# Kernel optimization log

Hardware: AMD Instinct MI355X
Metric: run time of the kernel (lower is better)

The kernel has to match this reference:

```python
import jax, jax.numpy as jnp
import numpy as np

D_MODEL = 1024
NUM_HEADS = 16
D_KEY = 64
CTX = 2048
B, T = 2, 2048


def setup_inputs() -> dict:
    key = jax.random.key(0)
    ks = jax.random.split(key, 5)
    scale_in = 1.0 / np.sqrt(D_MODEL)
    scale_out = 1.0 / np.sqrt(NUM_HEADS * D_KEY)
    return {
        "X": jax.random.normal(ks[0], (B, T, D_MODEL), dtype=jnp.float32),
        "Wqkv": jax.random.uniform(ks[1], (D_MODEL, 3 * NUM_HEADS * D_KEY), dtype=jnp.float32, minval=-scale_in, maxval=scale_in),
        "bqkv": jax.random.uniform(ks[2], (3 * NUM_HEADS * D_KEY,), dtype=jnp.float32, minval=-scale_in, maxval=scale_in),
        "Wout": jax.random.uniform(ks[3], (NUM_HEADS * D_KEY, D_MODEL), dtype=jnp.float32, minval=-scale_out, maxval=scale_out),
        "bout": jax.random.uniform(ks[4], (D_MODEL,), dtype=jnp.float32, minval=-scale_out, maxval=scale_out),
    }


def reference(X, Wqkv, bqkv, Wout, bout):
    b, t, _ = X.shape
    # project and split into q, k, v: [B,T,3,H,Dk]
    qkv = (X @ Wqkv + bqkv).reshape(b, t, 3, NUM_HEADS, D_KEY)
    q = qkv[:, :, 0].transpose(0, 2, 1, 3)  # [B,H,T,Dk]
    k = qkv[:, :, 1].transpose(0, 2, 1, 3)
    v = qkv[:, :, 2].transpose(0, 2, 1, 3)
    scores = jnp.einsum("bhqd,bhkd->bhqk", q, k) / jnp.sqrt(jnp.float32(D_KEY))
    causal = jnp.tril(jnp.ones((t, t), dtype=bool))  # [T,T]
    scores = jnp.where(causal, scores, -jnp.inf)
    attn = jax.nn.softmax(scores, axis=-1)
    out = jnp.einsum("bhqk,bhkd->bhqd", attn, v)  # [B,H,T,Dk]
    out = out.transpose(0, 2, 1, 3).reshape(b, t, NUM_HEADS * D_KEY)
    return out @ Wout + bout
```

## Files before the change

kernel.cpp:

```cpp
#include <hip/hip_runtime.h>
#include <hip/hip_bf16.h>
#include <math.h>

static constexpr int Bc = 2, Hc = 16, Tc = 2048, DKc = 64, DMc = 1024, NQKV = 3072;
#define QSCALE 0.18033688011112042f

typedef unsigned short u16;
typedef unsigned int u32;
typedef short s8v __attribute__((ext_vector_type(8)));
typedef float f32x4 __attribute__((ext_vector_type(4)));
typedef float f32x16 __attribute__((ext_vector_type(16)));
typedef int i32x4 __attribute__((ext_vector_type(4)));

#define DEVINL __device__ __forceinline__

DEVINL u16 f2b(float f) {
    union { float f; unsigned u; } v; v.f = f;
    unsigned u = v.u;
    unsigned r = (u + 0x7fffu + ((u >> 16) & 1u)) >> 16;
    return (u16)r;
}

DEVINL u32 pkbf16(float lo, float up) {
    u32 r;
    asm volatile("v_cvt_pk_bf16_f32 %0, %1, %2" : "=v"(r) : "v"(lo), "v"(up));
    return r;
}

DEVINL float vexp2(float x) {
    float r;
    asm("v_exp_f32 %0, %1" : "=v"(r) : "v"(x));
    return r;
}

DEVINL void pl32swap(u32& a, u32& b) {
    asm volatile("v_permlane32_swap_b32 %0, %1" : "+v"(a), "+v"(b));
}

DEVINL void gl_lds(const void* g, void* l) {
    __builtin_amdgcn_global_load_lds(
        (const __attribute__((address_space(1))) unsigned int*)g,
        (__attribute__((address_space(3))) unsigned int*)l, 16, 0, 0);
}

DEVINL s8v as_s8v(i32x4 x) { union { i32x4 i; s8v v; } u; u.i = x; return u.v; }

DEVINL void transw_tile(const float* __restrict__ W, u16* __restrict__ Wt,
                        int N, int K, int n0, int k0, u16 (*LT)[72], int t) {
    const int rr = t >> 4, cc = (t & 15) * 4;
    #pragma unroll
    for (int it = 0; it < 4; it++) {
        const int row = it * 16 + rr;
        float4 f = *(const float4*)&W[(size_t)(k0 + row) * N + n0 + cc];
        union { u16 u[4]; uint2 d; } o;
        o.u[0] = f2b(f.x); o.u[1] = f2b(f.y); o.u[2] = f2b(f.z); o.u[3] = f2b(f.w);
        *(uint2*)&LT[row][cc] = o.d;
    }
    __syncthreads();
    #pragma unroll
    for (int it = 0; it < 4; it++) {
        const int nrow = it * 16 + rr;
        union { u16 u[4]; uint2 d; } o;
        #pragma unroll
        for (int j = 0; j < 4; j++) o.u[j] = LT[cc + j][nrow];
        *(uint2*)&Wt[(size_t)(n0 + nrow) * K + k0 + cc] = o.d;
    }
}

__global__ __launch_bounds__(256) void prepass(
    const float* __restrict__ X, u16* __restrict__ Xb,
    const float* __restrict__ Wqkv, u16* __restrict__ Wt1,
    const float* __restrict__ Wout, u16* __restrict__ Wt2)
{
    __shared__ u16 LT[64][72];
    const int bid = blockIdx.x, t = threadIdx.x;
    if (bid < 1024) {
        const int n4 = (Bc * Tc * DMc) / 4;
        for (int i = bid * 256 + t; i < n4; i += 1024 * 256) {
            float4 f = ((const float4*)X)[i];
            union { u16 u[4]; uint2 d; } o;
            o.u[0] = f2b(f.x); o.u[1] = f2b(f.y); o.u[2] = f2b(f.z); o.u[3] = f2b(f.w);
            ((uint2*)Xb)[i] = o.d;
        }
    } else if (bid < 1024 + 768) {
        const int b2 = bid - 1024;
        transw_tile(Wqkv, Wt1, NQKV, DMc, (b2 % 48) * 64, (b2 / 48) * 64, LT, t);
    } else {
        const int b2 = bid - 1792;
        transw_tile(Wout, Wt2, DMc, DMc, (b2 % 16) * 64, (b2 / 16) * 64, LT, t);
    }
}

template <int EPI>
__global__ __launch_bounds__(512, 4) void gemm_ks(
    const u16* __restrict__ A, const u16* __restrict__ Bt,
    const float* __restrict__ bias,
    u16* __restrict__ q_out, u16* __restrict__ k_out, u16* __restrict__ v_out,
    float* __restrict__ f_out, int M, int N, int K, int ntn)
{
    __shared__ __align__(16) char Lds[70656];
    const int tid = threadIdx.x, lane = tid & 63, w = tid >> 6;
    const int qd = gridDim.x >> 3;
    const int wg = (blockIdx.x & 7) * qd + (blockIdx.x >> 3);
    const int m0 = (wg / ntn) * 128, n0 = (wg % ntn) * 128;
    const int g = w >> 2, sub = w & 3;
    const int wgm = sub >> 1, wgn = sub & 1;

    f32x4 acc[4][4] = {};
    const int R = K >> 6;

    const int srow = tid >> 2;
    const int skc  = ((tid & 3) ^ ((srow >> 1) & 3)) * 8;

#define STG2(j_) do {                                                          \
        const int ta_ = 2 * (j_), tb_ = ta_ + 1;                               \
        gl_lds(A  + (size_t)(m0 + srow) * K + ta_ * 32 + skc,                  \
               Lds + (ta_ & 3) * 8192 + w * 1024);                             \
        gl_lds(Bt + (size_t)(n0 + srow) * K + ta_ * 32 + skc,                  \
               Lds + 32768 + (ta_ & 3) * 8192 + w * 1024);                     \
        gl_lds(A  + (size_t)(m0 + srow) * K + tb_ * 32 + skc,                  \
               Lds + (tb_ & 3) * 8192 + w * 1024);                             \
        gl_lds(Bt + (size_t)(n0 + srow) * K + tb_ * 32 + skc,                  \
               Lds + 32768 + (tb_ & 3) * 8192 + w * 1024);                     \
    } while (0)
#define BARX() do { __builtin_amdgcn_sched_barrier(0);                         \
        __builtin_amdgcn_s_barrier();                                          \
        __builtin_amdgcn_sched_barrier(0); } while (0)

    STG2(0);
    for (int r = 0; r < R; ++r) {
        if (r + 1 < R) {
            STG2(r + 1);
            asm volatile("s_waitcnt vmcnt(4)" ::: "memory");
        } else {
            asm volatile("s_waitcnt vmcnt(0)" ::: "memory");
        }
        BARX();
        const int sl = (2 * r + g) & 3;
        const char* Abase = Lds + sl * 8192;
        const char* Bbase = Lds + 32768 + sl * 8192;
        s8v af[4], bf[4];
        #pragma unroll
        for (int mi = 0; mi < 4; mi++) {
            const int row = wgm * 64 + mi * 16 + (lane & 15);
            const int s16 = (lane >> 4) ^ ((row >> 1) & 3);
            af[mi] = *(const s8v*)(Abase + row * 64 + s16 * 16);
        }
        #pragma unroll
        for (int ni = 0; ni < 4; ni++) {
            const int row = wgn * 64 + ni * 16 + (lane & 15);
            const int s16 = (lane >> 4) ^ ((row >> 1) & 3);
            bf[ni] = *(const s8v*)(Bbase + row * 64 + s16 * 16);
        }
        __builtin_amdgcn_s_setprio(1);
        #pragma unroll
        for (int mi = 0; mi < 4; mi++)
            #pragma unroll
            for (int ni = 0; ni < 4; ni++)
                acc[mi][ni] = __builtin_amdgcn_mfma_f32_16x16x32_bf16(
                    af[mi], bf[ni], acc[mi][ni], 0, 0, 0);
        __builtin_amdgcn_s_setprio(0);
        BARX();
    }
#undef STG2
#undef BARX

    if (g == 1) {
        char* dst = Lds + sub * 17408 + lane * 272;
        #pragma unroll
        for (int mi = 0; mi < 4; mi++)
            #pragma unroll
            for (int ni = 0; ni < 4; ni++)
                *(f32x4*)(dst + (mi * 4 + ni) * 16) = acc[mi][ni];
    }
    __syncthreads();
    if (g == 0) {
        const char* src = Lds + sub * 17408 + lane * 272;
        #pragma unroll
        for (int mi = 0; mi < 4; mi++)
            #pragma unroll
            for (int ni = 0; ni < 4; ni++)
                acc[mi][ni] += *(const f32x4*)(src + (mi * 4 + ni) * 16);

        #pragma unroll
        for (int mi = 0; mi < 4; mi++)
        #pragma unroll
        for (int ni = 0; ni < 4; ni++)
        #pragma unroll
        for (int r = 0; r < 4; r++) {
            const int row = m0 + wgm * 64 + mi * 16 + (lane >> 4) * 4 + r;
            const int col = n0 + wgn * 64 + ni * 16 + (lane & 15);
            const float val = acc[mi][ni][r] + bias[col];
            if constexpr (EPI == 0) {
                const int sel = col >> 10, rem = col & 1023;
                const int h = rem >> 6, d = rem & 63;
                const int b = row >> 11, tt = row & 2047;
                const size_t idx = ((size_t)(b * Hc + h) * Tc + tt) * DKc + d;
                if (sel == 0) q_out[idx] = f2b(val * QSCALE);
                else if (sel == 1) k_out[idx] = f2b(val);
                else v_out[idx] = f2b(val);
            } else {
                f_out[(size_t)row * N + col] = val;
            }
        }
    }
}

template <int EPI>
__global__ __launch_bounds__(512) void gemm_cv(
    const u16* __restrict__ A, const u16* __restrict__ Bt,
    const float* __restrict__ bias,
    u16* __restrict__ q_out, u16* __restrict__ k_out, u16* __restrict__ v_out,
    float* __restrict__ f_out, int M, int N, int K, int ntn)
{
    __shared__ __align__(16) u16 Al[2][128 * 32];
    __shared__ __align__(16) u16 Bl[2][128 * 32];
    const int tid = threadIdx.x, lane = tid & 63, w = tid >> 6;
    const int qd = gridDim.x >> 3;
    const int wg = (blockIdx.x & 7) * qd + (blockIdx.x >> 3);
    const int m0 = (wg / ntn) * 128, n0 = (wg % ntn) * 128;
    const int wm = w >> 2, wn = w & 3;

    f32x4 acc[4][2] = {};
    const int nt = K >> 5;

    const int srow = tid >> 2;
    const int skc  = ((tid & 3) ^ ((srow >> 1) & 3)) * 8;

#define STG(t_, s_) do {                                                       \
        const int kk_ = (t_) << 5;                                             \
        gl_lds(A + (size_t)(m0 + srow) * K + kk_ + skc,                        \
               (char*)&Al[s_][0] + w * 1024);                                  \
        gl_lds(Bt + (size_t)(n0 + srow) * K + kk_ + skc,                       \
               (char*)&Bl[s_][0] + w * 1024);                                  \
    } while (0)
#define BARX() do { __builtin_amdgcn_sched_barrier(0);                         \
        __builtin_amdgcn_s_barrier();                                          \
        __builtin_amdgcn_sched_barrier(0); } while (0)

    STG(0, 0);
    int buf = 0;
    for (int t = 0; t < nt; t++) {
        if (t + 1 < nt) {
            STG(t + 1, buf ^ 1);
            asm volatile("s_waitcnt vmcnt(2)" ::: "memory");
        } else {
            asm volatile("s_waitcnt vmcnt(0)" ::: "memory");
        }
        BARX();
        s8v af[4], bf[2];
        #pragma unroll
        for (int mi = 0; mi < 4; mi++) {
            const int row = wm * 64 + mi * 16 + (lane & 15);
            const int slot = (lane >> 4) ^ ((row >> 1) & 3);
            af[mi] = *(const s8v*)((const char*)&Al[buf][0] + row * 64 + slot * 16);
        }
        #pragma unroll
        for (int ni = 0; ni < 2; ni++) {
            const int row = wn * 32 + ni * 16 + (lane & 15);
            const int slot = (lane >> 4) ^ ((row >> 1) & 3);
            bf[ni] = *(const s8v*)((const char*)&Bl[buf][0] + row * 64 + slot * 16);
        }
        #pragma unroll
        for (int mi = 0; mi < 4; mi++)
            #pragma unroll
            for (int ni = 0; ni < 2; ni++)
                acc[mi][ni] = __builtin_amdgcn_mfma_f32_16x16x32_bf16(af[mi], bf[ni], acc[mi][ni], 0, 0, 0);
        BARX();
        buf ^= 1;
    }
#undef STG
#undef BARX

    #pragma unroll
    for (int mi = 0; mi < 4; mi++)
    #pragma unroll
    for (int ni = 0; ni < 2; ni++)
    #pragma unroll
    for (int r = 0; r < 4; r++) {
        const int row = m0 + wm * 64 + mi * 16 + (lane >> 4) * 4 + r;
        const int col = n0 + wn * 32 + ni * 16 + (lane & 15);
        const float val = acc[mi][ni][r] + bias[col];
        if constexpr (EPI == 0) {
            const int sel = col >> 10, rem = col & 1023;
            const int h = rem >> 6, d = rem & 63;
            const int b = row >> 11, tt = row & 2047;
            const size_t idx = ((size_t)(b * Hc + h) * Tc + tt) * DKc + d;
            if (sel == 0) q_out[idx] = f2b(val * QSCALE);
            else if (sel == 1) k_out[idx] = f2b(val);
            else v_out[idx] = f2b(val);
        } else {
            f_out[(size_t)row * N + col] = val;
        }
    }
}

__global__ __launch_bounds__(512) void attn_fwd(
    const u16* __restrict__ Q, const u16* __restrict__ K,
    const u16* __restrict__ V, u16* __restrict__ O)
{
    __shared__ __align__(16) char Gl[2][2][2][8192];

    const int bid = blockIdx.x;
    const int bh = bid & 31;
    const int qt = 15 - (bid >> 5);
    const int tid = threadIdx.x;
    const int g = tid >> 8;
    const int gtid = tid & 255;
    const int lane = tid & 63;
    const int ws = (tid >> 6) & 3;
    const int hi = lane >> 5, lq = lane & 31;
    const int q0w = qt * 128 + ws * 32;
    const int qg = q0w + lq;

    const u16* Qb = Q + (size_t)bh * (Tc * DKc);
    const u16* Kb = K + (size_t)bh * (Tc * DKc);
    const u16* Vb = V + (size_t)bh * (Tc * DKc);

    s8v qf[4];
    #pragma unroll
    for (int st = 0; st < 4; st++)
        qf[st] = *(const s8v*)(Qb + (size_t)qg * 64 + st * 16 + hi * 8);

    f32x16 o0 = {}, o1 = {}, lacc = {};

    const int dtw = (q0w + 31) >> 6;
    const int h = qt + 1;
    const int t0 = g * h;

    char* const Kbase = &Gl[g][0][0][0];
    char* const Vbase = &Gl[g][1][0][0];

    const int d2 = (gtid & 31) * 2, kb8 = gtid >> 5;
    const unsigned vsw0 = ((unsigned)(d2 & 7)) << 4;
    const unsigned vsw1 = ((unsigned)((d2 + 1) & 7)) << 4;
    const unsigned ksw = ((unsigned)(lq & 7)) << 4;

    u32 vx[8];

#define ISSUE_K(kt_, dst_) do {                                              \
        const char* Ktile_ = (const char*)(Kb + (size_t)(kt_) * 4096);       \
        _Pragma("unroll")                                                    \
        for (int s_ = 0; s_ < 2; s_++) {                                     \
            const int o_ = s_ * 4096 + gtid * 16;                            \
            const int rk_ = o_ >> 7;                                         \
            const int cb_ = (o_ & 127) ^ ((rk_ & 7) << 4);                   \
            gl_lds(Ktile_ + rk_ * 128 + cb_, (dst_) + s_ * 4096 + ws * 1024); \
        }                                                                    \
    } while (0)

#define LOAD_V(kt_) do {                                                     \
        const u16* Vtile_ = Vb + (size_t)(kt_) * 4096;                       \
        _Pragma("unroll")                                                    \
        for (int i_ = 0; i_ < 8; i_++)                                       \
            vx[i_] = *(const u32*)(Vtile_ + (kb8 * 8 + i_) * 64 + d2);       \
    } while (0)

#define WRITE_V(dst_) do {                                                   \
        s8v v0_, v1_;                                                        \
        _Pragma("unroll")                                                    \
        for (int i_ = 0; i_ < 8; i_++) {                                     \
            v0_[i_] = (short)(vx[i_] & 0xffff);                              \
            v1_[i_] = (short)(vx[i_] >> 16);                                 \
        }                                                                    \
        *(s8v*)((dst_) + d2 * 128 + (((unsigned)(kb8 * 16)) ^ vsw0)) = v0_;  \
        *(s8v*)((dst_) + (d2 + 1) * 128 + (((unsigned)(kb8 * 16)) ^ vsw1)) = v1_; \
    } while (0)

    ISSUE_K(t0, Kbase);
    LOAD_V(t0);
    WRITE_V(Vbase);
    __syncthreads();

    int c = 0;
    for (int i = 0; i < h; i++) {
        const int tki = t0 + i;
        const bool pf_next = (i + 1 < h);
        if (pf_next) {
            ISSUE_K(tki + 1, Kbase + (c ^ 1) * 8192);
            LOAD_V(tki + 1);
        }

        if (tki <= dtw) {
            const char* Kc = Kbase + c * 8192;
            const char* Vc = Vbase + c * 8192;
            f32x16 s0v = {}, s1v = {};
            __builtin_amdgcn_s_setprio(1);
            #pragma unroll
            for (int st = 0; st < 4; st++) {
                const unsigned cbs = (unsigned)(st * 32 + hi * 16);
                s8v kf0 = *(const s8v*)(Kc + lq * 128 + (cbs ^ ksw));
                s8v kf1 = *(const s8v*)(Kc + (32 + lq) * 128 + (cbs ^ ksw));
                s0v = __builtin_amdgcn_mfma_f32_32x32x16_bf16(kf0, qf[st], s0v, 0, 0, 0);
                s1v = __builtin_amdgcn_mfma_f32_32x32x16_bf16(kf1, qf[st], s1v, 0, 0, 0);
            }
            __builtin_amdgcn_s_setprio(0);

            if (tki == dtw) {
                #pragma unroll
                for (int r = 0; r < 16; r++) {
                    const int kg = tki * 64 + (r & 3) + 8 * (r >> 2) + 4 * hi;
                    if (kg > qg) s0v[r] = -INFINITY;
                    if (kg + 32 > qg) s1v[r] = -INFINITY;
                }
            }

            #pragma unroll
            for (int r = 0; r < 16; r++) {
                s0v[r] = vexp2(s0v[r]);
                s1v[r] = vexp2(s1v[r]);
            }
            lacc += s0v;
            lacc += s1v;

            i32x4 pf[4];
            #pragma unroll
            for (int gq = 0; gq < 2; gq++) {
                #pragma unroll
                for (int hq = 0; hq < 2; hq++) {
                    const int base = hq * 8;
                    u32 a0, a1, b0, b1;
                    if (gq == 0) {
                        a0 = pkbf16(s0v[base + 0], s0v[base + 1]);
                        a1 = pkbf16(s0v[base + 2], s0v[base + 3]);
                        b0 = pkbf16(s0v[base + 4], s0v[base + 5]);
                        b1 = pkbf16(s0v[base + 6], s0v[base + 7]);
                    } else {
                        a0 = pkbf16(s1v[base + 0], s1v[base + 1]);
                        a1 = pkbf16(s1v[base + 2], s1v[base + 3]);
                        b0 = pkbf16(s1v[base + 4], s1v[base + 5]);
                        b1 = pkbf16(s1v[base + 6], s1v[base + 7]);
                    }
                    pl32swap(a0, b0);
                    pl32swap(a1, b1);
                    pf[gq * 2 + hq][0] = (int)a0;
                    pf[gq * 2 + hq][1] = (int)a1;
                    pf[gq * 2 + hq][2] = (int)b0;
                    pf[gq * 2 + hq][3] = (int)b1;
                }
            }

            __builtin_amdgcn_s_setprio(1);
            #pragma unroll
            for (int ks = 0; ks < 4; ks++) {
                const unsigned cbv = (unsigned)(ks * 32 + hi * 16);
                s8v vf0 = *(const s8v*)(Vc + lq * 128 + (cbv ^ ksw));
                s8v vf1 = *(const s8v*)(Vc + (32 + lq) * 128 + (cbv ^ ksw));
                const s8v pa = as_s8v(pf[ks]);
                o0 = __builtin_amdgcn_mfma_f32_32x32x16_bf16(pa, vf0, o0, 0, 0, 0);
                o1 = __builtin_amdgcn_mfma_f32_32x32x16_bf16(pa, vf1, o1, 0, 0, 0);
            }
            __builtin_amdgcn_s_setprio(0);
        }

        if (pf_next) WRITE_V(Vbase + (c ^ 1) * 8192);
        __syncthreads();
        c ^= 1;
    }

    float t8[8];
    #pragma unroll
    for (int r = 0; r < 8; r++) t8[r] = lacc[r] + lacc[r + 8];
    #pragma unroll
    for (int off = 4; off >= 1; off >>= 1)
        #pragma unroll
        for (int r = 0; r < off; r++) t8[r] = t8[r] + t8[r + off];
    float ls = t8[0] + __shfl_xor(t8[0], 32);

    float* Pf = (float*)(&Gl[0][0][0][0]) + ws * 2304;
    if (g == 1) {
        float* dst = Pf + lane * 34;
        #pragma unroll
        for (int r = 0; r < 16; r++) { dst[r] = o0[r]; dst[16 + r] = o1[r]; }
        Pf[2176 + lane] = ls;
    }
    __syncthreads();
    if (g == 0) {
        const float* src = Pf + lane * 34;
        #pragma unroll
        for (int r = 0; r < 16; r++) { o0[r] += src[r]; o1[r] += src[16 + r]; }
        ls += Pf[2176 + lane];

        const float linv = 1.0f / ls;
        const int b = bh >> 4, hh = bh & 15;
        u16* Ob = O + ((size_t)b * Tc) * DMc + hh * 64;
        #pragma unroll
        for (int r = 0; r < 16; r++) {
            const int cr = (r & 3) + 8 * (r >> 2) + 4 * hi;
            const float ir = __shfl(linv, cr);
            u16* orow = Ob + (size_t)(q0w + cr) * DMc;
            orow[lq]      = f2b(o0[r] * ir);
            orow[32 + lq] = f2b(o1[r] * ir);
        }
    }
#undef ISSUE_K
#undef LOAD_V
#undef WRITE_V
}

extern "C" void kernel_launch(void* const* d_in, const int* in_sizes, int n_in,
                              void* d_out, int out_size, void* d_ws, size_t ws_size,
                              hipStream_t stream)
{
    const float* X    = (const float*)d_in[0];
    const float* Wqkv = (const float*)d_in[1];
    const float* bqkv = (const float*)d_in[2];
    const float* Wout = (const float*)d_in[3];
    const float* bout = (const float*)d_in[4];
    float* out = (float*)d_out;

    char* ws = (char*)d_ws;
    u16* Xb  = (u16*)(ws);
    u16* Ow  = (u16*)(ws);
    u16* Wt1 = (u16*)(ws + (8 << 20));
    u16* Wt2 = (u16*)(ws + (14 << 20));
    u16* Qw  = (u16*)(ws + (16 << 20));
    u16* Kw  = (u16*)(ws + (24 << 20));
    u16* Vw  = (u16*)(ws + (32 << 20));

    prepass<<<2048, 256, 0, stream>>>(X, Xb, Wqkv, Wt1, Wout, Wt2);

    gemm_ks<0><<<768, 512, 0, stream>>>(
        Xb, Wt1, bqkv, Qw, Kw, Vw, nullptr, Bc * Tc, NQKV, DMc, NQKV / 128);

    attn_fwd<<<512, 512, 0, stream>>>(Qw, Kw, Vw, Ow);

    gemm_cv<1><<<256, 512, 0, stream>>>(
        Ow, Wt2, bout, nullptr, nullptr, nullptr, out, Bc * Tc, DMc, DMc, DMc / 128);
}
```

Measured before the change: 107.7 us.

## Shrink QKV GEMM LDS footprint with two-slot ping-pong and halved split-K reduction

The QKV projection GEMM changes from a four-slot LDS ring, where both wave groups compute every step, to a two-slot buffer of 32-wide K tiles. Each wave group handles alternating tiles, so every iteration has one group idle and the loop runs twice as many barriers. The cross-group split-K reduction now happens in two halves, reusing the smaller LDS buffer. LDS drops from about 69KB to 32KB, which allows more resident blocks per CU, but the explicit minimum-occupancy launch bound is removed and per-iteration compute density falls.

```diff
diff --git a/kernel.cpp b/kernel.cpp
--- a/kernel.cpp
+++ b/kernel.cpp
@@ -92,13 +92,13 @@
 }
 
 template <int EPI>
-__global__ __launch_bounds__(512, 4) void gemm_ks(
+__global__ __launch_bounds__(512) void gemm_kp(
     const u16* __restrict__ A, const u16* __restrict__ Bt,
     const float* __restrict__ bias,
     u16* __restrict__ q_out, u16* __restrict__ k_out, u16* __restrict__ v_out,
     float* __restrict__ f_out, int M, int N, int K, int ntn)
 {
-    __shared__ __align__(16) char Lds[70656];
+    __shared__ __align__(16) char Lds[32768];
     const int tid = threadIdx.x, lane = tid & 63, w = tid >> 6;
     const int qd = gridDim.x >> 3;
     const int wg = (blockIdx.x & 7) * qd + (blockIdx.x >> 3);
@@ -107,81 +107,84 @@
     const int wgm = sub >> 1, wgn = sub & 1;
 
     f32x4 acc[4][4] = {};
-    const int R = K >> 6;
+    const int nt = K >> 5;
 
     const int srow = tid >> 2;
     const int skc  = ((tid & 3) ^ ((srow >> 1) & 3)) * 8;
 
-#define STG2(j_) do {                                                          \
-        const int ta_ = 2 * (j_), tb_ = ta_ + 1;                               \
-        gl_lds(A  + (size_t)(m0 + srow) * K + ta_ * 32 + skc,                  \
-               Lds + (ta_ & 3) * 8192 + w * 1024);                             \
-        gl_lds(Bt + (size_t)(n0 + srow) * K + ta_ * 32 + skc,                  \
-               Lds + 32768 + (ta_ & 3) * 8192 + w * 1024);                     \
-        gl_lds(A  + (size_t)(m0 + srow) * K + tb_ * 32 + skc,                  \
-               Lds + (tb_ & 3) * 8192 + w * 1024);                             \
-        gl_lds(Bt + (size_t)(n0 + srow) * K + tb_ * 32 + skc,                  \
-               Lds + 32768 + (tb_ & 3) * 8192 + w * 1024);                     \
+#define STG(t_) do {                                                           \
+        const int s_ = (t_) & 1;                                               \
+        gl_lds(A + (size_t)(m0 + srow) * K + ((t_) << 5) + skc,                \
+               Lds + s_ * 8192 + w * 1024);                                    \
+        gl_lds(Bt + (size_t)(n0 + srow) * K + ((t_) << 5) + skc,               \
+               Lds + 16384 + s_ * 8192 + w * 1024);                            \
     } while (0)
 #define BARX() do { __builtin_amdgcn_sched_barrier(0);                         \
         __builtin_amdgcn_s_barrier();                                          \
         __builtin_amdgcn_sched_barrier(0); } while (0)
 
-    STG2(0);
-    for (int r = 0; r < R; ++r) {
-        if (r + 1 < R) {
-            STG2(r + 1);
-            asm volatile("s_waitcnt vmcnt(4)" ::: "memory");
+    STG(0);
+    for (int t = 0; t < nt; t++) {
+        if (t + 1 < nt) {
+            STG(t + 1);
+            asm volatile("s_waitcnt vmcnt(2)" ::: "memory");
         } else {
             asm volatile("s_waitcnt vmcnt(0)" ::: "memory");
         }
         BARX();
-        const int sl = (2 * r + g) & 3;
-        const char* Abase = Lds + sl * 8192;
-        const char* Bbase = Lds + 32768 + sl * 8192;
-        s8v af[4], bf[4];
-        #pragma unroll
-        for (int mi = 0; mi < 4; mi++) {
-            const int row = wgm * 64 + mi * 16 + (lane & 15);
-            const int s16 = (lane >> 4) ^ ((row >> 1) & 3);
-            af[mi] = *(const s8v*)(Abase + row * 64 + s16 * 16);
-        }
-        #pragma unroll
-        for (int ni = 0; ni < 4; ni++) {
-            const int row = wgn * 64 + ni * 16 + (lane & 15);
-            const int s16 = (lane >> 4) ^ ((row >> 1) & 3);
-            bf[ni] = *(const s8v*)(Bbase + row * 64 + s16 * 16);
-        }
-        __builtin_amdgcn_s_setprio(1);
-        #pragma unroll
-        for (int mi = 0; mi < 4; mi++)
-            #pragma unroll
-            for (int ni = 0; ni < 4; ni++)
-                acc[mi][ni] = __builtin_amdgcn_mfma_f32_16x16x32_bf16(
-                    af[mi], bf[ni], acc[mi][ni], 0, 0, 0);
-        __builtin_amdgcn_s_setprio(0);
+        if ((t & 1) == g) {
+            const char* Ab = Lds + g * 8192;
+            const char* Bb = Lds + 16384 + g * 8192;
+            s8v af[4], bf[4];
+            #pragma unroll
+            for (int mi = 0; mi < 4; mi++) {
+                const int row = wgm * 64 + mi * 16 + (lane & 15);
+                const int s16 = (lane >> 4) ^ ((row >> 1) & 3);
+                af[mi] = *(const s8v*)(Ab + row * 64 + s16 * 16);
+            }
+            #pragma unroll
+            for (int ni = 0; ni < 4; ni++) {
+                const int row = wgn * 64 + ni * 16 + (lane & 15);
+                const int s16 = (lane >> 4) ^ ((row >> 1) & 3);
+                bf[ni] = *(const s8v*)(Bb + row * 64 + s16 * 16);
+            }
+            __builtin_amdgcn_s_setprio(1);
+            #pragma unroll
+            for (int mi = 0; mi < 4; mi++)
+                #pragma unroll
+                for (int ni = 0; ni < 4; ni++)
+                    acc[mi][ni] = __builtin_amdgcn_mfma_f32_16x16x32_bf16(
+                        af[mi], bf[ni], acc[mi][ni], 0, 0, 0);
+            __builtin_amdgcn_s_setprio(0);
+        }
         BARX();
     }
-#undef STG2
+#undef STG
 #undef BARX
 
-    if (g == 1) {
-        char* dst = Lds + sub * 17408 + lane * 272;
-        #pragma unroll
-        for (int mi = 0; mi < 4; mi++)
-            #pragma unroll
-            for (int ni = 0; ni < 4; ni++)
-                *(f32x4*)(dst + (mi * 4 + ni) * 16) = acc[mi][ni];
-    }
-    __syncthreads();
+    #pragma unroll
+    for (int half = 0; half < 2; half++) {
+        if (g == 1) {
+            char* dst = Lds + sub * 8192;
+            #pragma unroll
+            for (int mi = 0; mi < 2; mi++)
+                #pragma unroll
+                for (int ni = 0; ni < 4; ni++)
+                    *(f32x4*)(dst + (mi * 4 + ni) * 1024 + lane * 16) = acc[half * 2 + mi][ni];
+        }
+        __syncthreads();
+        if (g == 0) {
+            const char* src = Lds + sub * 8192;
+            #pragma unroll
+            for (int mi = 0; mi < 2; mi++)
+                #pragma unroll
+                for (int ni = 0; ni < 4; ni++)
+                    acc[half * 2 + mi][ni] += *(const f32x4*)(src + (mi * 4 + ni) * 1024 + lane * 16);
+        }
+        __syncthreads();
+    }
+
     if (g == 0) {
-        const char* src = Lds + sub * 17408 + lane * 272;
-        #pragma unroll
-        for (int mi = 0; mi < 4; mi++)
-            #pragma unroll
-            for (int ni = 0; ni < 4; ni++)
-                acc[mi][ni] += *(const f32x4*)(src + (mi * 4 + ni) * 16);
-
         #pragma unroll
         for (int mi = 0; mi < 4; mi++)
         #pragma unroll
@@ -520,7 +523,7 @@
 
     prepass<<<2048, 256, 0, stream>>>(X, Xb, Wqkv, Wt1, Wout, Wt2);
 
-    gemm_ks<0><<<768, 512, 0, stream>>>(
+    gemm_kp<0><<<768, 512, 0, stream>>>(
         Xb, Wt1, bqkv, Qw, Kw, Vw, nullptr, Bc * Tc, NQKV, DMc, NQKV / 128);
 
     attn_fwd<<<512, 512, 0, stream>>>(Qw, Kw, Vw, Ow);
```

New measurement: 108.2 us. About the same (+0.5%).
